# Optimization experiments

Measured on AMD Instinct MI355X. Metric: run time of the kernel, lower is better.

The kernel has to match this reference:

```python
import jax, jax.numpy as jnp
import numpy as np

EMBED_DIM = 1024
NUM_HEADS = 16
HEAD_DIM = EMBED_DIM // NUM_HEADS
N, S = 4, 8192


def setup_inputs() -> dict:
    key = jax.random.key(0)
    ks = jax.random.split(key, 9)
    sc = 1.0 / np.sqrt(EMBED_DIM)
    d = {"x": jax.random.normal(ks[0], (N, S, EMBED_DIM), dtype=jnp.float32)}
    for i, name in enumerate(["Wq", "Wk", "Wv", "Wo"]):
        d[name] = jax.random.normal(ks[1 + i], (EMBED_DIM, EMBED_DIM), dtype=jnp.float32) * sc
    for i, name in enumerate(["bq", "bk", "bv", "bo"]):
        d[name] = jax.random.normal(ks[5 + i], (EMBED_DIM,), dtype=jnp.float32) * 0.01
    return d


def reference(x, Wq, Wk, Wv, Wo, bq, bk, bv, bo):
    n, s, e = x.shape
    # projections: nn.Linear => x @ W.T + b
    Q = x @ Wq.T + bq
    K = x @ Wk.T + bk
    V = x @ Wv.T + bv
    # (N, S, H, D) -> (N, H, S, D), matching torch .view().transpose(1, 2)
    Q = Q.reshape(n, s, NUM_HEADS, HEAD_DIM).transpose(0, 2, 1, 3)
    K = K.reshape(n, s, NUM_HEADS, HEAD_DIM).transpose(0, 2, 1, 3)
    V = V.reshape(n, s, NUM_HEADS, HEAD_DIM).transpose(0, 2, 1, 3)
    # Faithful to the original (buggy) einsum labeling: on (N,H,S,D) tensors
    # 'nqhd,nkhd->nhqk' attends OVER THE HEAD AXIS -> energy (N, S, H, H)
    energy = jnp.einsum('nqhd,nkhd->nhqk', Q, K)
    attention = jax.nn.softmax(energy / jnp.sqrt(jnp.float32(e)), axis=3)
    # out: (N, H, S, D), then reshaped as if (N, S, H*D) — exact original math
    out = jnp.einsum('nhql,nlhd->nqhd', attention, V).reshape(n, s, e)
    return out @ Wo.T + bo
```

## Files before the change

kernel.cpp:

```cpp
#include <hip/hip_runtime.h>
#include <cstdint>
#include <cstddef>

typedef unsigned short u16;
typedef __attribute__((ext_vector_type(8))) __bf16 bf16x8;
typedef __attribute__((ext_vector_type(4))) float floatx4;

typedef const __attribute__((address_space(1))) void* gptr_t;
typedef __attribute__((address_space(3))) void* lptr_t;

__device__ __forceinline__ u16 f2b(float f) {
    unsigned u = __builtin_bit_cast(unsigned, f);
    u += 0x7fffu + ((u >> 16) & 1u);
    return (u16)(u >> 16);
}

__global__ void cast_f32_bf16(const float* __restrict__ in, u16* __restrict__ out, int n4) {
    int i = blockIdx.x * blockDim.x + threadIdx.x;
    if (i < n4) {
        const float4 v = ((const float4*)in)[i];
        ushort4 o;
        o.x = f2b(v.x); o.y = f2b(v.y); o.z = f2b(v.z); o.w = f2b(v.w);
        ((ushort4*)out)[i] = o;
    }
}

template <bool OUT_BF16>
__global__ __launch_bounds__(256, 2)
void gemm_bt(const u16* __restrict__ A, const u16* __restrict__ B,
             const float* __restrict__ bias, void* __restrict__ Cout,
             int N, int K)
{
    __shared__ u16 lA[128 * 32];
    __shared__ u16 lB[128 * 32];

    const int tid  = threadIdx.x;
    const int m0   = blockIdx.y * 128;
    const int n0   = blockIdx.x * 128;
    const int row  = tid >> 2;
    const int chk  = tid & 3;
    const int lane = tid & 63;
    const int wv   = tid >> 6;
    const int wm   = wv >> 1;
    const int wn   = wv & 1;
    const int lrow = lane & 15;
    const int quad = lane >> 4;

    const u16* gA0 = A + (size_t)(m0 + row) * K + chk * 8;
    const u16* gB0 = B + (size_t)(n0 + row) * K + chk * 8;
    u16* sA0 = lA + tid * 8;
    u16* sB0 = lB + tid * 8;

    const u16* pA = lA + (wm * 64 + lrow) * 32 + quad * 8;
    const u16* pB = lB + (wn * 64 + lrow) * 32 + quad * 8;

    const floatx4 fzero = {0.f, 0.f, 0.f, 0.f};
    floatx4 acc[4][4];
    #pragma unroll
    for (int i = 0; i < 4; i++)
        #pragma unroll
        for (int j = 0; j < 4; j++) acc[i][j] = fzero;

    const size_t rstride = (size_t)64 * K;

    for (int k0 = 0; k0 < K; k0 += 32) {
        __builtin_amdgcn_global_load_lds((gptr_t)(gA0 + k0),           (lptr_t)sA0,          16, 0, 0);
        __builtin_amdgcn_global_load_lds((gptr_t)(gA0 + rstride + k0), (lptr_t)(sA0 + 2048), 16, 0, 0);
        __builtin_amdgcn_global_load_lds((gptr_t)(gB0 + k0),           (lptr_t)sB0,          16, 0, 0);
        __builtin_amdgcn_global_load_lds((gptr_t)(gB0 + rstride + k0), (lptr_t)(sB0 + 2048), 16, 0, 0);
        __syncthreads();

        bf16x8 af[4], bfr[4];
        #pragma unroll
        for (int i = 0; i < 4; i++) {
            af[i]  = *(const bf16x8*)(pA + i * 512);
            bfr[i] = *(const bf16x8*)(pB + i * 512);
        }
        #pragma unroll
        for (int i = 0; i < 4; i++)
            #pragma unroll
            for (int j = 0; j < 4; j++)
                acc[i][j] = __builtin_amdgcn_mfma_f32_16x16x32_bf16(af[i], bfr[j], acc[i][j], 0, 0, 0);
        __syncthreads();
    }

    float bsv[4];
    #pragma unroll
    for (int j = 0; j < 4; j++) bsv[j] = bias[n0 + wn * 64 + j * 16 + lrow];

    #pragma unroll
    for (int i = 0; i < 4; i++) {
        const int mbase = m0 + wm * 64 + i * 16 + quad * 4;
        #pragma unroll
        for (int j = 0; j < 4; j++) {
            const int n = n0 + wn * 64 + j * 16 + lrow;
            #pragma unroll
            for (int r = 0; r < 4; r++) {
                const float v = acc[i][j][r] + bsv[j];
                const size_t idx = (size_t)(mbase + r) * N + n;
                if constexpr (OUT_BF16) ((u16*)Cout)[idx] = f2b(v);
                else                    ((float*)Cout)[idx] = v;
            }
        }
    }
}

__global__ __launch_bounds__(256)
void attn(const u16* __restrict__ QKV, u16* __restrict__ Z)
{
    __shared__ u16 sA[4][16 * 32];
    const int lane = threadIdx.x & 63;
    const int wv   = threadIdx.x >> 6;
    const int lrow = lane & 15;
    const int quad = lane >> 4;
    const int tok  = blockIdx.x * 4 + wv;

    const u16* base = QKV + (size_t)tok * 3072;

    for (int idx = lane; idx < 256; idx += 64)
        sA[wv][(idx >> 4) * 32 + 16 + (idx & 15)] = 0;

    const bf16x8 q0 = *(const bf16x8*)(base + lrow * 64 + quad * 8);
    const bf16x8 q1 = *(const bf16x8*)(base + lrow * 64 + 32 + quad * 8);
    const bf16x8 k0 = *(const bf16x8*)(base + 1024 + lrow * 64 + quad * 8);
    const bf16x8 k1 = *(const bf16x8*)(base + 1024 + lrow * 64 + 32 + quad * 8);

    const floatx4 fzero = {0.f, 0.f, 0.f, 0.f};
    floatx4 e = fzero;
    e = __builtin_amdgcn_mfma_f32_16x16x32_bf16(q0, k0, e, 0, 0, 0);
    e = __builtin_amdgcn_mfma_f32_16x16x32_bf16(q1, k1, e, 0, 0, 0);

    #pragma unroll
    for (int r = 0; r < 4; r++) {
        float xv = e[r] * 0.03125f;
        float mx = xv;
        mx = fmaxf(mx, __shfl_xor(mx, 1));
        mx = fmaxf(mx, __shfl_xor(mx, 2));
        mx = fmaxf(mx, __shfl_xor(mx, 4));
        mx = fmaxf(mx, __shfl_xor(mx, 8));
        float p = __expf(xv - mx);
        float s = p;
        s += __shfl_xor(s, 1);
        s += __shfl_xor(s, 2);
        s += __shfl_xor(s, 4);
        s += __shfl_xor(s, 8);
        sA[wv][(quad * 4 + r) * 32 + lrow] = f2b(p / s);
    }
    __syncthreads();

    const bf16x8 afrag = *(const bf16x8*)(&sA[wv][lrow * 32 + quad * 8]);

    bf16x8 vf[4];
    #pragma unroll
    for (int j = 0; j < 4; j++)
        #pragma unroll
        for (int jj = 0; jj < 8; jj++)
            vf[j][jj] = __builtin_bit_cast(__bf16, (u16)0);
    if (quad < 2) {
        const u16* V = base + 2048;
        #pragma unroll
        for (int j = 0; j < 4; j++)
            #pragma unroll
            for (int jj = 0; jj < 8; jj++)
                vf[j][jj] = __builtin_bit_cast(__bf16, V[(quad * 8 + jj) * 64 + j * 16 + lrow]);
    }

    const int nb = tok >> 13;
    const int sl = tok & 8191;
    const size_t zbase = ((size_t)nb * 8192 + (sl >> 4)) * 1024 + (size_t)(sl & 15) * 64;
    #pragma unroll
    for (int j = 0; j < 4; j++) {
        floatx4 y = __builtin_amdgcn_mfma_f32_16x16x32_bf16(afrag, vf[j], fzero, 0, 0, 0);
        #pragma unroll
        for (int r = 0; r < 4; r++)
            Z[zbase + (size_t)(quad * 4 + r) * 512 * 1024 + j * 16 + lrow] = f2b(y[r]);
    }
}

extern "C" void kernel_launch(void* const* d_in, const int* in_sizes, int n_in,
                              void* d_out, int out_size, void* d_ws, size_t ws_size,
                              hipStream_t stream)
{
    (void)in_sizes; (void)n_in; (void)out_size;
    const float* x  = (const float*)d_in[0];
    const float* Wq = (const float*)d_in[1];
    const float* Wk = (const float*)d_in[2];
    const float* Wv = (const float*)d_in[3];
    const float* Wo = (const float*)d_in[4];
    const float* bq = (const float*)d_in[5];
    const float* bk = (const float*)d_in[6];
    const float* bv = (const float*)d_in[7];
    const float* bo = (const float*)d_in[8];

    const size_t Mtot = 32768;
    char* ws = (char*)d_ws;
    u16*   Xbf  = (u16*)ws;
    u16*   Wqkv = (u16*)(ws + (64ull << 20));
    u16*   Wob  = (u16*)(ws + (64ull << 20) + (6ull << 20));
    float* bqkv = (float*)(ws + (72ull << 20));
    char*  dyn  = ws + (72ull << 20) + 16384;
    const size_t fixed = (72ull << 20) + 16384;

    int c = 4;
    for (int cc = 1; cc <= 4; cc <<= 1) {
        size_t Rr = Mtot / cc;
        if (fixed + Rr * 3072 * 2 + Rr * 1024 * 2 <= ws_size) { c = cc; break; }
    }
    const size_t R = Mtot / c;
    u16* QKV = (u16*)dyn;
    u16* Zb  = (u16*)(dyn + R * 3072 * 2);

    cast_f32_bf16<<<dim3(32768), dim3(256), 0, stream>>>(x, Xbf, (int)(Mtot * 1024 / 4));
    cast_f32_bf16<<<dim3(1024),  dim3(256), 0, stream>>>(Wq, Wqkv,           262144);
    cast_f32_bf16<<<dim3(1024),  dim3(256), 0, stream>>>(Wk, Wqkv + 1048576, 262144);
    cast_f32_bf16<<<dim3(1024),  dim3(256), 0, stream>>>(Wv, Wqkv + 2097152, 262144);
    cast_f32_bf16<<<dim3(1024),  dim3(256), 0, stream>>>(Wo, Wob,            262144);
    hipMemcpyAsync(bqkv,        bq, 1024 * sizeof(float), hipMemcpyDeviceToDevice, stream);
    hipMemcpyAsync(bqkv + 1024, bk, 1024 * sizeof(float), hipMemcpyDeviceToDevice, stream);
    hipMemcpyAsync(bqkv + 2048, bv, 1024 * sizeof(float), hipMemcpyDeviceToDevice, stream);

    for (int ci = 0; ci < c; ci++) {
        const u16* Ab   = Xbf + (size_t)ci * R * 1024;
        float*     outp = (float*)d_out + (size_t)ci * R * 1024;
        gemm_bt<true ><<<dim3(3072 / 128, (unsigned)(R / 128)), dim3(256), 0, stream>>>(Ab, Wqkv, bqkv, QKV, 3072, 1024);
        attn<<<dim3((unsigned)(R / 4)), dim3(256), 0, stream>>>(QKV, Zb);
        gemm_bt<false><<<dim3(1024 / 128, (unsigned)(R / 128)), dim3(256), 0, stream>>>(Zb, Wob, bo, outp, 1024, 1024);
    }
}
```

Before: 648.5 us.

## Batch 16 tokens per attn block and coalesce V loads and Z stores via LDS

The attention kernel now handles 16 consecutive tokens per block (4 per wave). V is loaded with vectorized 16-byte reads and transposed through LDS instead of scalar strided gathers. Outputs are staged in an LDS tile and written to Z as contiguous 16-byte rows, replacing scattered 2-byte stores. The cost is more LDS per block and a serial per-wave token loop, which may reduce occupancy.

```diff
diff --git a/kernel.cpp b/kernel.cpp
--- a/kernel.cpp
+++ b/kernel.cpp
@@ -108,72 +108,106 @@
 __global__ __launch_bounds__(256)
 void attn(const u16* __restrict__ QKV, u16* __restrict__ Z)
 {
-    __shared__ u16 sA[4][16 * 32];
-    const int lane = threadIdx.x & 63;
-    const int wv   = threadIdx.x >> 6;
+    __shared__ __align__(16) u16 sV[4][1024];
+    __shared__ __align__(16) u16 sA[4][640];
+    __shared__ __align__(16) u16 sY[16 * 1152];
+
+    const int tid  = threadIdx.x;
+    const int lane = tid & 63;
+    const int wv   = tid >> 6;
     const int lrow = lane & 15;
     const int quad = lane >> 4;
-    const int tok  = blockIdx.x * 4 + wv;
-
-    const u16* base = QKV + (size_t)tok * 3072;
-
-    for (int idx = lane; idx < 256; idx += 64)
-        sA[wv][(idx >> 4) * 32 + 16 + (idx & 15)] = 0;
-
-    const bf16x8 q0 = *(const bf16x8*)(base + lrow * 64 + quad * 8);
-    const bf16x8 q1 = *(const bf16x8*)(base + lrow * 64 + 32 + quad * 8);
-    const bf16x8 k0 = *(const bf16x8*)(base + 1024 + lrow * 64 + quad * 8);
-    const bf16x8 k1 = *(const bf16x8*)(base + 1024 + lrow * 64 + 32 + quad * 8);
+    const int pp   = lane >> 3;
+    const int cc   = lane & 7;
+
+    #pragma unroll
+    for (int i = 0; i < 4; i++) {
+        const int idx = i * 64 + lane;
+        sA[wv][(idx >> 4) * 40 + 16 + (idx & 15)] = 0;
+    }
+
+    const int tgrp = blockIdx.x * 16;
+    const int nb   = tgrp >> 13;
+    const int sg   = (tgrp & 8191) >> 4;
 
     const floatx4 fzero = {0.f, 0.f, 0.f, 0.f};
-    floatx4 e = fzero;
-    e = __builtin_amdgcn_mfma_f32_16x16x32_bf16(q0, k0, e, 0, 0, 0);
-    e = __builtin_amdgcn_mfma_f32_16x16x32_bf16(q1, k1, e, 0, 0, 0);
-
-    #pragma unroll
-    for (int r = 0; r < 4; r++) {
-        float xv = e[r] * 0.03125f;
-        float mx = xv;
-        mx = fmaxf(mx, __shfl_xor(mx, 1));
-        mx = fmaxf(mx, __shfl_xor(mx, 2));
-        mx = fmaxf(mx, __shfl_xor(mx, 4));
-        mx = fmaxf(mx, __shfl_xor(mx, 8));
-        float p = __expf(xv - mx);
-        float s = p;
-        s += __shfl_xor(s, 1);
-        s += __shfl_xor(s, 2);
-        s += __shfl_xor(s, 4);
-        s += __shfl_xor(s, 8);
-        sA[wv][(quad * 4 + r) * 32 + lrow] = f2b(p / s);
-    }
+
+    for (int tt = 0; tt < 4; tt++) {
+        const int t = wv * 4 + tt;
+        const u16* base = QKV + (size_t)(tgrp + t) * 3072;
+
+        const bf16x8 q0 = *(const bf16x8*)(base + lrow * 64      + quad * 8);
+        const bf16x8 q1 = *(const bf16x8*)(base + lrow * 64 + 32 + quad * 8);
+        const bf16x8 k0 = *(const bf16x8*)(base + 1024 + lrow * 64      + quad * 8);
+        const bf16x8 k1 = *(const bf16x8*)(base + 1024 + lrow * 64 + 32 + quad * 8);
+
+        const u16* V = base + 2048;
+        const bf16x8 va = *(const bf16x8*)(V + (2 * pp)     * 64 + cc * 8);
+        const bf16x8 vb = *(const bf16x8*)(V + (2 * pp + 1) * 64 + cc * 8);
+        #pragma unroll
+        for (int s = 0; s < 8; s++) {
+            const unsigned pv = (unsigned)__builtin_bit_cast(u16, (__bf16)va[s]) |
+                                ((unsigned)__builtin_bit_cast(u16, (__bf16)vb[s]) << 16);
+            *(unsigned*)&sV[wv][(s * 8 + cc) * 16 + 2 * pp] = pv;
+        }
+
+        floatx4 e = fzero;
+        e = __builtin_amdgcn_mfma_f32_16x16x32_bf16(q0, k0, e, 0, 0, 0);
+        e = __builtin_amdgcn_mfma_f32_16x16x32_bf16(q1, k1, e, 0, 0, 0);
+
+        #pragma unroll
+        for (int r = 0; r < 4; r++) {
+            const float xv = e[r] * 0.03125f;
+            float mx = xv;
+            mx = fmaxf(mx, __shfl_xor(mx, 1));
+            mx = fmaxf(mx, __shfl_xor(mx, 2));
+            mx = fmaxf(mx, __shfl_xor(mx, 4));
+            mx = fmaxf(mx, __shfl_xor(mx, 8));
+            const float p = __expf(xv - mx);
+            float s = p;
+            s += __shfl_xor(s, 1);
+            s += __shfl_xor(s, 2);
+            s += __shfl_xor(s, 4);
+            s += __shfl_xor(s, 8);
+            sA[wv][(quad * 4 + r) * 40 + lrow] = f2b(p / s);
+        }
+
+        const bf16x8 af = *(const bf16x8*)&sA[wv][lrow * 40 + quad * 8];
+
+        bf16x8 bfr[4];
+        #pragma unroll
+        for (int j = 0; j < 4; j++)
+            #pragma unroll
+            for (int jj = 0; jj < 8; jj++)
+                bfr[j][jj] = __builtin_bit_cast(__bf16, (u16)0);
+        if (quad < 2) {
+            #pragma unroll
+            for (int j = 0; j < 4; j++) {
+                const int pr = (lrow & 7) * 8 + j * 2 + (lrow >> 3);
+                bfr[j] = *(const bf16x8*)&sV[wv][pr * 16 + quad * 8];
+            }
+        }
+
+        #pragma unroll
+        for (int j = 0; j < 4; j++) {
+            const floatx4 y = __builtin_amdgcn_mfma_f32_16x16x32_bf16(af, bfr[j], fzero, 0, 0, 0);
+            #pragma unroll
+            for (int r = 0; r < 4; r++)
+                sY[t * 1152 + (quad * 4 + r) * 72 + j * 16 + lrow] = f2b(y[r]);
+        }
+    }
+
     __syncthreads();
 
-    const bf16x8 afrag = *(const bf16x8*)(&sA[wv][lrow * 32 + quad * 8]);
-
-    bf16x8 vf[4];
-    #pragma unroll
-    for (int j = 0; j < 4; j++)
-        #pragma unroll
-        for (int jj = 0; jj < 8; jj++)
-            vf[j][jj] = __builtin_bit_cast(__bf16, (u16)0);
-    if (quad < 2) {
-        const u16* V = base + 2048;
-        #pragma unroll
-        for (int j = 0; j < 4; j++)
-            #pragma unroll
-            for (int jj = 0; jj < 8; jj++)
-                vf[j][jj] = __builtin_bit_cast(__bf16, V[(quad * 8 + jj) * 64 + j * 16 + lrow]);
-    }
-
-    const int nb = tok >> 13;
-    const int sl = tok & 8191;
-    const size_t zbase = ((size_t)nb * 8192 + (sl >> 4)) * 1024 + (size_t)(sl & 15) * 64;
-    #pragma unroll
-    for (int j = 0; j < 4; j++) {
-        floatx4 y = __builtin_amdgcn_mfma_f32_16x16x32_bf16(afrag, vf[j], fzero, 0, 0, 0);
-        #pragma unroll
-        for (int r = 0; r < 4; r++)
-            Z[zbase + (size_t)(quad * 4 + r) * 512 * 1024 + j * 16 + lrow] = f2b(y[r]);
+    const int h   = tid >> 4;
+    const int pos = tid & 15;
+    u16* zrow = Z + (size_t)(nb * 8192 + h * 512 + sg) * 1024;
+    #pragma unroll
+    for (int it = 0; it < 8; it++) {
+        const int c16 = it * 16 + pos;
+        const int t = c16 >> 3, dc = c16 & 7;
+        const uint4 v = *(const uint4*)&sY[t * 1152 + h * 72 + dc * 8];
+        *(uint4*)(zrow + c16 * 8) = v;
     }
 }
 
@@ -223,7 +257,7 @@
         const u16* Ab   = Xbf + (size_t)ci * R * 1024;
         float*     outp = (float*)d_out + (size_t)ci * R * 1024;
         gemm_bt<true ><<<dim3(3072 / 128, (unsigned)(R / 128)), dim3(256), 0, stream>>>(Ab, Wqkv, bqkv, QKV, 3072, 1024);
-        attn<<<dim3((unsigned)(R / 4)), dim3(256), 0, stream>>>(QKV, Zb);
+        attn<<<dim3((unsigned)(R / 16)), dim3(256), 0, stream>>>(QKV, Zb);
         gemm_bt<false><<<dim3(1024 / 128, (unsigned)(R / 128)), dim3(256), 0, stream>>>(Zb, Wob, bo, outp, 1024, 1024);
     }
 }
```

Measured after the change: 621.0 us. -4.2%, faster.
